# Kernel optimization log

Hardware: AMD Instinct MI355X
Metric: run time of the kernel (lower is better)

## Reference

```python
import jax, jax.numpy as jnp
import numpy as np

N_TAPS = 5
N_DELAY = 1
N_ITER = 2
REF_MIC = 0
EPS = 1e-3        # eps passed to ISS updates / divisions
MODEL_EPS = 1e-5  # LaplaceModel internal eps
PB_EPS = 1e-6     # projection_back eps


def _mag_sq(x):
    return jnp.real(x) ** 2 + jnp.imag(x) ** 2


def _div(num, den, eps=EPS):
    # torchiva divide: num / clamp(den, min=eps); den is real
    return num / jnp.maximum(den, eps)


def _laplace_model(Y):
    # Laplace source model: per-source/per-frame weight 1/(2*||y(:,n)||), broadcast over freq
    denom = 2.0 * jnp.sqrt(jnp.sum(_mag_sq(Y), axis=-2, keepdims=True))
    return jnp.broadcast_to(1.0 / jnp.maximum(denom, MODEL_EPS), Y.shape)


def _demix_derev(X, X_bar, W, H):
    reverb = jnp.einsum('...cfdt,...dftn->...cfn', H, X_bar)
    sep = jnp.einsum('...cfd,...dfn->...cfn', W, X)
    return sep - reverb


def _background_update(W, H, C_XX, C_XbarX):
    n_src = W.shape[-3]
    A = (jnp.einsum('...sfc,...cfd->...fsd', W, C_XX)
         + jnp.einsum('...sfdt,...dtfc->...fsc', H, C_XbarX))
    J_H = jnp.linalg.solve(A[..., :n_src], A[..., n_src:])  # (..., f, s, c-s)
    return jnp.moveaxis(jnp.conj(J_H), -1, -3)              # (..., c-s, f, s)


def _demix_background(X, J):
    n_src = J.shape[-1]
    return jnp.einsum('...cfd,...dfn->...cfn', J, X[..., :n_src, :, :]) - X[..., n_src:, :, :]


def _iss_v1(src, X, weights, eps=EPS):
    n_frames = X.shape[-1]
    Xs = X[..., src, :, :]
    v_num = jnp.einsum('...cfn,...cfn,...fn->...cf', weights, X, jnp.conj(Xs)) / n_frames
    v_den = jnp.einsum('...cfn,...fn->...cf', weights, _mag_sq(Xs)) / n_frames
    v = _div(v_num, v_den, eps)
    v_s = 1.0 - 1.0 / jnp.sqrt(jnp.maximum(v_den[..., src, :], eps))
    return v.at[..., src, :].set(v_s.astype(v.dtype))


def _iss_v23(X, Zs, weights, eps=EPS):
    v_num = jnp.einsum('...cfn,...cfn,...fn->...cf', weights, X, jnp.conj(Zs))
    v_den = jnp.einsum('...cfn,...fn->...cf', weights, _mag_sq(Zs))
    return _div(v_num, v_den, eps)


def _iss_updates_with_H(X, X_bar, W, H, weights, J=None, Z=None, eps=EPS):
    n_src = X.shape[-3]
    n_chan = n_src if J is None else n_src + Z.shape[-3]
    n_taps = X_bar.shape[-2]
    # sequential rank-1 source updates (loop-carried; small fixed trip count)
    for src in range(n_src):
        v = _iss_v1(src, X, weights, eps)
        X = X - jnp.einsum('...cf,...fn->...cfn', v, X[..., src, :, :])
        W = W - jnp.einsum('...cf,...fd->...cfd', v, W[..., src, :, :])
        H = H - jnp.einsum('...cf,...fdt->...cfdt', v, H[..., src, :, :, :])
    if Z is not None and J is not None:
        for bak in range(n_chan - n_src):
            v = _iss_v23(X, Z[..., bak, :, :], weights, eps)
            X = X - jnp.einsum('...cf,...fn->...cfn', v, Z[..., bak, :, :])
            W = W.at[..., :n_src].add(-jnp.einsum('...cf,...fd->...cfd', v, J[..., bak, :, :]))
            W = W.at[..., n_src + bak].add(v)
    for src in range(n_chan):
        for tap in range(n_taps):
            Xst = X_bar[..., src, :, tap, :]
            v = _iss_v23(X, Xst, weights, eps)
            X = X - jnp.einsum('...cf,...fn->...cfn', v, Xst)
            H = H.at[..., src, tap].add(v)
    return X, W, H


def _one_iter(Y, X, X_bar, C_XX, C_XbarX, W, H, J, eps=EPS):
    weights = _laplace_model(Y)
    g = jnp.maximum(jnp.mean(_mag_sq(Y), axis=(-2, -1), keepdims=True), eps)
    g_sqrt = jnp.sqrt(g)
    Y = _div(Y, g_sqrt, eps)
    W = _div(W, g_sqrt, eps)
    H = _div(H, g_sqrt[..., None], eps)
    weights = weights * g
    J = _background_update(W, H, C_XX, C_XbarX)
    Z = _demix_background(X, J)
    Y, W, H = _iss_updates_with_H(Y, X_bar, W, H, weights, J=J, Z=Z, eps=eps)
    return Y, W, H, J


def _projection_back(Y, W, J, ref_mic=REF_MIC, eps=PB_EPS):
    # overdetermined branch (n_src < n_chan), ref_mic < n_src
    n_src = Y.shape[-3]
    eye = jnp.eye(n_src, dtype=W.dtype)
    W1, W2 = W[..., :n_src], W[..., n_src:]
    B = jnp.einsum('...sfc,...cfk->...sfk', W2, J) + W1  # (..., s, f, s)
    rhs = eye[:, ref_mic:ref_mic + 1]                    # (s, 1)
    BT = jnp.einsum('...sfc->...fcs', B)                 # (..., f, s, s)
    rhs_b = jnp.broadcast_to(rhs, BT.shape[:-2] + rhs.shape)
    a = jnp.linalg.solve(BT + eps * eye, rhs_b)          # (..., f, s, 1)
    a = jnp.swapaxes(a, -3, -2)                          # (..., s, f, 1)
    return Y * a


def _forward(X, n_src):
    n_chan, n_freq, n_frames = X.shape[-3:]
    batch = X.shape[:-3]
    # delayed copies: X_bar[..., c, f, t, n] = X_pad[..., c, f, n + t]
    X_pad = jnp.pad(X, [(0, 0)] * (X.ndim - 1) + [(N_TAPS + N_DELAY, 0)])
    X_bar = jnp.stack([X_pad[..., t:t + n_frames] for t in range(N_TAPS)], axis=-2)
    C_XX = jnp.einsum('...cfn,...dfn->...cfd', X, jnp.conj(X)) / n_frames
    C_XbarX = jnp.einsum('...dftn,...cfn->...dtfc', X_bar, jnp.conj(X)) / n_frames
    eye = jnp.eye(n_chan, dtype=X.dtype)[:n_src]
    W = jnp.broadcast_to(eye[:, None, :], batch + (n_src, n_freq, n_chan))
    H = jnp.zeros(batch + (n_src, n_freq, n_chan, N_TAPS), dtype=X.dtype)
    J = jnp.zeros(batch + (n_chan - n_src, n_freq, n_src), dtype=X.dtype)
    Y = X[..., :n_src, :, :]
    for _ in range(N_ITER):
        Y, W, H, J = _one_iter(Y, X, X_bar, C_XX, C_XbarX, W, H, J)
    J = _background_update(W, H, C_XX, C_XbarX)
    Y = _demix_derev(X, X_bar, W, H)
    Y = _projection_back(Y, W, J)
    return Y


def setup_inputs():
    key = jax.random.key(0)
    k1, k2 = jax.random.split(key)
    B, n_chan, n_freq, n_frames = 2, 6, 257, 1000
    X_real = jax.random.normal(k1, (B, n_chan, n_freq, n_frames), dtype=jnp.float32)
    X_imag = jax.random.normal(k2, (B, n_chan, n_freq, n_frames), dtype=jnp.float32)
    return {"X_real": X_real, "X_imag": X_imag, "n_src": 2}


def reference(X_real, X_imag, n_src):
    X = jax.lax.complex(X_real, X_imag)
    Y = _forward(X, n_src)  # (B, n_src, n_freq, n_frames) complex
    # real view of the complex output: last axis = (real, imag)
    return jnp.stack([jnp.real(Y), jnp.imag(Y)], axis=-1)
```

## Files before the change

### kernel.cpp

```cpp
#include <hip/hip_runtime.h>
#include <math.h>

#define F_   257
#define N_   1000
#define C_   6
#define S_   2
#define K_   4
#define T_   5
#define DLY  6
#define EPSF 1e-3f
#define MODEL_EPSF 1e-5f
#define PB_EPSD 1e-6
#define NTHR 512

__device__ __forceinline__ float2 cmul(float2 a, float2 b){
  return make_float2(a.x*b.x - a.y*b.y, a.x*b.y + a.y*b.x);
}
__device__ __forceinline__ float2 cadd(float2 a, float2 b){ return make_float2(a.x+b.x, a.y+b.y); }
__device__ __forceinline__ float2 csub(float2 a, float2 b){ return make_float2(a.x-b.x, a.y-b.y); }

struct dc { double x, y; };
__device__ __forceinline__ dc dmul(dc a, dc b){ return dc{a.x*b.x - a.y*b.y, a.x*b.y + a.y*b.x}; }
__device__ __forceinline__ dc dadd(dc a, dc b){ return dc{a.x+b.x, a.y+b.y}; }
__device__ __forceinline__ dc dsub(dc a, dc b){ return dc{a.x-b.x, a.y-b.y}; }
__device__ __forceinline__ dc ddiv(dc a, dc b){
  double d = b.x*b.x + b.y*b.y;
  return dc{(a.x*b.x + a.y*b.y)/d, (a.y*b.x - a.x*b.y)/d};
}
__device__ __forceinline__ dc d_of(float2 a){ return dc{(double)a.x, (double)a.y}; }

struct V2 { float2 v0, v1; };

__global__ __launch_bounds__(512) void k_init(const float* __restrict__ Xre,
    const float* __restrict__ Xim, float2* __restrict__ Cxxg, float2* __restrict__ Cbxg)
{
  __shared__ float2 Xl[C_*N_];
  int p = blockIdx.x; int b = p / F_; int f = p - b*F_;
  int tid = threadIdx.x;

  for (int i = tid; i < C_*N_; i += NTHR){
    int c = i / N_, n = i - c*N_;
    size_t gi = ((size_t)(b*C_+c)*F_ + f)*N_ + n;
    Xl[i] = make_float2(Xre[gi], Xim[gi]);
  }
  __syncthreads();

  int wid = tid >> 6, lane = tid & 63;
  const float inv_n = 1.0f / (float)N_;
  for (int e = wid; e < 216; e += 8){
    int a_ch, b_ch, lag; float2* outp;
    if (e < 36){
      a_ch = e / 6; b_ch = e - a_ch*6; lag = 0;
      outp = &Cxxg[((size_t)p*C_ + a_ch)*C_ + b_ch];
    } else {
      int i2 = e - 36;
      int d = i2 / (T_*C_); int t = (i2 / C_) % T_; int c2 = i2 % C_;
      a_ch = d; b_ch = c2; lag = DLY - t;
      outp = &Cbxg[(((size_t)p*C_ + d)*T_ + t)*C_ + c2];
    }
    float accx = 0.f, accy = 0.f;
    for (int n = lane; n < N_; n += 64){
      if (n >= lag){
        float2 xa = Xl[a_ch*N_ + n - lag];
        float2 xb = Xl[b_ch*N_ + n];
        accx += xa.x*xb.x + xa.y*xb.y;
        accy += xa.y*xb.x - xa.x*xb.y;
      }
    }
    #pragma unroll
    for (int off = 32; off; off >>= 1){
      accx += __shfl_xor(accx, off);
      accy += __shfl_xor(accy, off);
    }
    if (lane == 0) *outp = make_float2(accx*inv_n, accy*inv_n);
  }
}

__global__ __launch_bounds__(128) void k_weights_x(const float* __restrict__ Xre,
    const float* __restrict__ Xim, float* __restrict__ deng, float* __restrict__ gsumg)
{
  __shared__ float redw[2];
  int blk = blockIdx.x;
  int fc = blk & 3; int ch = (blk >> 2) & 7; int s = (blk >> 5) & 1; int b = blk >> 6;
  int tid = threadIdx.x;
  int n = ch*125 + tid;
  int f0 = fc*65, f1 = (f0 + 65 < F_) ? f0 + 65 : F_;
  float acc = 0.f;
  if (tid < 125){
    for (int f = f0; f < f1; ++f){
      size_t gi = ((size_t)(b*C_+s)*F_ + f)*N_ + n;
      float xr = Xre[gi], xi = Xim[gi];
      acc += xr*xr + xi*xi;
    }
    atomicAdd(&deng[(b*S_+s)*N_ + n], acc);
  }
  float r = (tid < 125) ? acc : 0.f;
  #pragma unroll
  for (int off = 32; off; off >>= 1) r += __shfl_xor(r, off);
  if ((tid & 63) == 0) redw[tid >> 6] = r;
  __syncthreads();
  if (tid == 0) atomicAdd(&gsumg[b*S_+s], redw[0] + redw[1]);
}

__global__ __launch_bounds__(128) void k_weights_y(const float2* __restrict__ Yg,
    float* __restrict__ deng, float* __restrict__ gsumg)
{
  __shared__ float redw[2];
  int blk = blockIdx.x;
  int fc = blk & 3; int ch = (blk >> 2) & 7; int s = (blk >> 5) & 1; int b = blk >> 6;
  int tid = threadIdx.x;
  int n = ch*125 + tid;
  int f0 = fc*65, f1 = (f0 + 65 < F_) ? f0 + 65 : F_;
  float acc = 0.f;
  if (tid < 125){
    for (int f = f0; f < f1; ++f){
      float2 y = Yg[(((size_t)(b*F_+f))*S_ + s)*N_ + n];
      acc += y.x*y.x + y.y*y.y;
    }
    atomicAdd(&deng[(b*S_+s)*N_ + n], acc);
  }
  float r = (tid < 125) ? acc : 0.f;
  #pragma unroll
  for (int off = 32; off; off >>= 1) r += __shfl_xor(r, off);
  if ((tid & 63) == 0) redw[tid >> 6] = r;
  __syncthreads();
  if (tid == 0) atomicAdd(&gsumg[b*S_+s], redw[0] + redw[1]);
}

__device__ __forceinline__ void bg_update(int tid, int p, const float2* Wl,
    const float2* Hl, float2* Al, float2* Jl,
    const float2* __restrict__ Cxxg, const float2* __restrict__ Cbxg)
{
  if (tid < S_*C_){
    int s = tid / C_, j = tid - s*C_;
    float2 a = make_float2(0.f, 0.f);
    const float2* cx = Cxxg + (size_t)p*C_*C_;
    #pragma unroll
    for (int i = 0; i < C_; ++i) a = cadd(a, cmul(Wl[s*C_+i], cx[i*C_+j]));
    const float2* cb = Cbxg + (size_t)p*C_*T_*C_;
    #pragma unroll
    for (int i = 0; i < C_; ++i)
      #pragma unroll
      for (int t = 0; t < T_; ++t)
        a = cadd(a, cmul(Hl[(s*C_+i)*T_+t], cb[(i*T_+t)*C_+j]));
    Al[s*C_+j] = a;
  }
  __syncthreads();
  if (tid == 0){
    dc M00 = d_of(Al[0]),  M01 = d_of(Al[1]);
    dc M10 = d_of(Al[C_]), M11 = d_of(Al[C_+1]);
    dc det = dsub(dmul(M00, M11), dmul(M01, M10));
    #pragma unroll
    for (int k = 0; k < K_; ++k){
      dc r0 = d_of(Al[2+k]), r1 = d_of(Al[C_+2+k]);
      dc x0 = ddiv(dsub(dmul(M11, r0), dmul(M01, r1)), det);
      dc x1 = ddiv(dsub(dmul(M00, r1), dmul(M10, r0)), det);
      Jl[k*S_+0] = make_float2((float)x0.x, (float)(-x0.y));
      Jl[k*S_+1] = make_float2((float)x1.x, (float)(-x1.y));
    }
  }
  __syncthreads();
}

template<typename FS>
__device__ __forceinline__ V2 round2(int tid, bool hasB, int rb, float2* redv,
    float2& yA0, float2& yA1, float2& yB0, float2& yB1,
    float wA0, float wA1, float wB0, float wB1,
    FS sf, bool isV1, int src)
{
  float2 sA = sf(0), sB = sf(1);
  float m = sA.x*sA.x + sA.y*sA.y;
  float r0 = wA0*(yA0.x*sA.x + yA0.y*sA.y);
  float r1 = wA0*(yA0.y*sA.x - yA0.x*sA.y);
  float r2 = wA0*m;
  float r3 = wA1*(yA1.x*sA.x + yA1.y*sA.y);
  float r4 = wA1*(yA1.y*sA.x - yA1.x*sA.y);
  float r5 = wA1*m;
  if (hasB){
    float mb = sB.x*sB.x + sB.y*sB.y;
    r0 += wB0*(yB0.x*sB.x + yB0.y*sB.y);
    r1 += wB0*(yB0.y*sB.x - yB0.x*sB.y);
    r2 += wB0*mb;
    r3 += wB1*(yB1.x*sB.x + yB1.y*sB.y);
    r4 += wB1*(yB1.y*sB.x - yB1.x*sB.y);
    r5 += wB1*mb;
  }
  #pragma unroll
  for (int off = 32; off; off >>= 1){
    r0 += __shfl_xor(r0, off); r1 += __shfl_xor(r1, off);
    r2 += __shfl_xor(r2, off); r3 += __shfl_xor(r3, off);
    r4 += __shfl_xor(r4, off); r5 += __shfl_xor(r5, off);
  }
  if ((tid & 63) == 0){
    float2* rw = redv + rb*24 + (tid >> 6)*3;
    rw[0] = make_float2(r0, r1);
    rw[1] = make_float2(r2, r3);
    rw[2] = make_float2(r4, r5);
  }
  __syncthreads();
  const float2* rp = redv + rb*24;
  float t0=0,t1=0,t2=0,t3=0,t4=0,t5=0;
  #pragma unroll
  for (int w = 0; w < 8; ++w){
    float2 a = rp[w*3], b2 = rp[w*3+1], c2 = rp[w*3+2];
    t0 += a.x; t1 += a.y; t2 += b2.x; t3 += b2.y; t4 += c2.x; t5 += c2.y;
  }
  if (isV1){
    const float inv = 1.f/(float)N_;
    t0*=inv; t1*=inv; t2*=inv; t3*=inv; t4*=inv; t5*=inv;
  }
  float d0 = fmaxf(t2, EPSF), d1 = fmaxf(t5, EPSF);
  float2 v0 = make_float2(t0/d0, t1/d0);
  float2 v1 = make_float2(t3/d1, t4/d1);
  if (isV1){
    if (src == 0) v0 = make_float2(1.f - 1.f/sqrtf(d0), 0.f);
    else          v1 = make_float2(1.f - 1.f/sqrtf(d1), 0.f);
  }
  yA0 = csub(yA0, cmul(v0, sA)); yA1 = csub(yA1, cmul(v1, sA));
  if (hasB){ yB0 = csub(yB0, cmul(v0, sB)); yB1 = csub(yB1, cmul(v1, sB)); }
  return V2{v0, v1};
}

template<bool FIRST, bool FINAL>
__global__ __launch_bounds__(512, 4) void k_main(const float* __restrict__ Xre,
    const float* __restrict__ Xim, float2* __restrict__ Yg, float2* __restrict__ Wg,
    float2* __restrict__ Hg, const float2* __restrict__ Cxxg,
    const float2* __restrict__ Cbxg, const float* __restrict__ deng,
    const float* __restrict__ gsumg, float2* __restrict__ out2, int P)
{
  __shared__ float2 Xl[C_*N_];
  __shared__ float2 Wl[S_*C_];
  __shared__ float2 Hl[S_*C_*T_];
  __shared__ float2 Jl[K_*S_];
  __shared__ float2 Al[S_*C_];
  __shared__ float2 redv[2*8*3];

  int tid = threadIdx.x;
  const int nA = tid;
  const int nB = tid + NTHR;
  const bool hasB = (nB < N_);
  const int nBs = hasB ? nB : 0;

  for (int p = blockIdx.x; p < P; p += gridDim.x){
    __syncthreads();
    int b = p / F_, f = p - b*F_;

    for (int i = tid; i < C_*N_; i += NTHR){
      int c = i / N_, n = i - c*N_;
      size_t gi = ((size_t)(b*C_+c)*F_ + f)*N_ + n;
      Xl[i] = make_float2(Xre[gi], Xim[gi]);
    }

    float gv0 = fmaxf(gsumg[b*S_+0] * (1.f/((float)F_*(float)N_)), EPSF);
    float gv1 = fmaxf(gsumg[b*S_+1] * (1.f/((float)F_*(float)N_)), EPSF);
    float ig0 = 1.f / fmaxf(sqrtf(gv0), EPSF);
    float ig1 = 1.f / fmaxf(sqrtf(gv1), EPSF);

    float wA0 = gv0 / fmaxf(2.f*sqrtf(deng[(b*S_+0)*N_+nA]), MODEL_EPSF);
    float wA1 = gv1 / fmaxf(2.f*sqrtf(deng[(b*S_+1)*N_+nA]), MODEL_EPSF);
    float wB0 = 0.f, wB1 = 0.f;
    if (hasB){
      wB0 = gv0 / fmaxf(2.f*sqrtf(deng[(b*S_+0)*N_+nB]), MODEL_EPSF);
      wB1 = gv1 / fmaxf(2.f*sqrtf(deng[(b*S_+1)*N_+nB]), MODEL_EPSF);
    }

    if (FIRST){
      if (tid < S_*C_){
        int s = tid / C_, c = tid - s*C_;
        Wl[tid] = make_float2((s==c) ? (s ? ig1 : ig0) : 0.f, 0.f);
      }
      if (tid < S_*C_*T_) Hl[tid] = make_float2(0.f, 0.f);
    } else {
      if (tid < S_*C_){
        float ig = (tid / C_) ? ig1 : ig0;
        float2 w = Wg[(size_t)p*S_*C_ + tid];
        Wl[tid] = make_float2(w.x*ig, w.y*ig);
      }
      if (tid < S_*C_*T_){
        float ig = (tid / (C_*T_)) ? ig1 : ig0;
        float2 h = Hg[(size_t)p*S_*C_*T_ + tid];
        Hl[tid] = make_float2(h.x*ig, h.y*ig);
      }
    }
    __syncthreads();

    float2 xA0 = Xl[nA], xA1 = Xl[N_+nA];
    float2 xB0 = make_float2(0.f,0.f), xB1 = make_float2(0.f,0.f);
    if (hasB){ xB0 = Xl[nB]; xB1 = Xl[N_+nB]; }

    float2 yA0, yA1, yB0 = make_float2(0.f,0.f), yB1 = make_float2(0.f,0.f);
    if (FIRST){
      yA0 = make_float2(xA0.x*ig0, xA0.y*ig0);
      yA1 = make_float2(xA1.x*ig1, xA1.y*ig1);
      if (hasB){
        yB0 = make_float2(xB0.x*ig0, xB0.y*ig0);
        yB1 = make_float2(xB1.x*ig1, xB1.y*ig1);
      }
    } else {
      float2 t0 = Yg[((size_t)p*S_+0)*N_+nA];
      float2 t1 = Yg[((size_t)p*S_+1)*N_+nA];
      yA0 = make_float2(t0.x*ig0, t0.y*ig0);
      yA1 = make_float2(t1.x*ig1, t1.y*ig1);
      if (hasB){
        float2 u0 = Yg[((size_t)p*S_+0)*N_+nB];
        float2 u1 = Yg[((size_t)p*S_+1)*N_+nB];
        yB0 = make_float2(u0.x*ig0, u0.y*ig0);
        yB1 = make_float2(u1.x*ig1, u1.y*ig1);
      }
    }

    bg_update(tid, p, Wl, Hl, Al, Jl, Cxxg, Cbxg);

    int rr = 0;

    for (int src2 = 0; src2 < S_; ++src2){
      V2 v = round2(tid, hasB, (rr++)&1, redv, yA0,yA1,yB0,yB1, wA0,wA1,wB0,wB1,
          [&](int k)->float2 {
            return (src2 == 0) ? (k ? yB0 : yA0) : (k ? yB1 : yA1);
          }, true, src2);
      if (tid < C_){
        float2 ws = Wl[src2*C_+tid];
        Wl[tid]      = csub(Wl[tid],      cmul(v.v0, ws));
        Wl[C_+tid]   = csub(Wl[C_+tid],   cmul(v.v1, ws));
      } else if (tid >= 64 && tid < 64 + C_*T_){
        int i = tid - 64;
        float2 hs = Hl[src2*C_*T_+i];
        Hl[i]        = csub(Hl[i],        cmul(v.v0, hs));
        Hl[C_*T_+i]  = csub(Hl[C_*T_+i],  cmul(v.v1, hs));
      }
    }

    for (int bak = 0; bak < K_; ++bak){
      float2 J0 = Jl[bak*S_+0], J1 = Jl[bak*S_+1];
      V2 v = round2(tid, hasB, (rr++)&1, redv, yA0,yA1,yB0,yB1, wA0,wA1,wB0,wB1,
          [&](int k)->float2 {
            float2 x0 = k ? xB0 : xA0;
            float2 x1 = k ? xB1 : xA1;
            int n = k ? nBs : nA;
            float2 z = cadd(cmul(J0, x0), cmul(J1, x1));
            return csub(z, Xl[(S_+bak)*N_ + n]);
          }, false, 0);
      if (tid < S_){
        float2 vv = tid ? v.v1 : v.v0;
        Wl[tid*C_+0]      = csub(Wl[tid*C_+0], cmul(vv, J0));
        Wl[tid*C_+1]      = csub(Wl[tid*C_+1], cmul(vv, J1));
        Wl[tid*C_+S_+bak] = cadd(Wl[tid*C_+S_+bak], vv);
      }
    }

    for (int sc = 0; sc < C_; ++sc){
      for (int tap = 0; tap < T_; ++tap){
        int lag = DLY - tap;
        V2 v = round2(tid, hasB, (rr++)&1, redv, yA0,yA1,yB0,yB1, wA0,wA1,wB0,wB1,
            [&](int k)->float2 {
              int n = (k ? nBs : nA) - lag;
              return (n >= 0) ? Xl[sc*N_ + n] : make_float2(0.f, 0.f);
            }, false, 0);
        if (tid < S_){
          int idx = (tid*C_+sc)*T_+tap;
          Hl[idx] = cadd(Hl[idx], tid ? v.v1 : v.v0);
        }
      }
    }

    __syncthreads();

    if (!FINAL){
      Yg[((size_t)p*S_+0)*N_+nA] = yA0;
      Yg[((size_t)p*S_+1)*N_+nA] = yA1;
      if (hasB){
        Yg[((size_t)p*S_+0)*N_+nB] = yB0;
        Yg[((size_t)p*S_+1)*N_+nB] = yB1;
      }
      if (tid < S_*C_)    Wg[(size_t)p*S_*C_ + tid]    = Wl[tid];
      if (tid < S_*C_*T_) Hg[(size_t)p*S_*C_*T_ + tid] = Hl[tid];
    } else {
      bg_update(tid, p, Wl, Hl, Al, Jl, Cxxg, Cbxg);

      float2 oA0 = make_float2(0.f,0.f), oA1 = oA0, oB0 = oA0, oB1 = oA0;
      #pragma unroll
      for (int d = 0; d < C_; ++d){
        float2 x = Xl[d*N_+nA];
        oA0 = cadd(oA0, cmul(Wl[d],    x));
        oA1 = cadd(oA1, cmul(Wl[C_+d], x));
      }
      #pragma unroll
      for (int t = 0; t < T_; ++t){
        int m = nA - (DLY - t);
        if (m >= 0){
          #pragma unroll
          for (int d = 0; d < C_; ++d){
            float2 x = Xl[d*N_+m];
            oA0 = csub(oA0, cmul(Hl[d*T_+t],        x));
            oA1 = csub(oA1, cmul(Hl[(C_+d)*T_+t],   x));
          }
        }
      }
      if (hasB){
        #pragma unroll
        for (int d = 0; d < C_; ++d){
          float2 x = Xl[d*N_+nB];
          oB0 = cadd(oB0, cmul(Wl[d],    x));
          oB1 = cadd(oB1, cmul(Wl[C_+d], x));
        }
        #pragma unroll
        for (int t = 0; t < T_; ++t){
          int m = nB - (DLY - t);
          #pragma unroll
          for (int d = 0; d < C_; ++d){
            float2 x = Xl[d*N_+m];
            oB0 = csub(oB0, cmul(Hl[d*T_+t],      x));
            oB1 = csub(oB1, cmul(Hl[(C_+d)*T_+t], x));
          }
        }
      }

      if (tid == 0){
        dc Bm[2][2];
        #pragma unroll
        for (int s2 = 0; s2 < S_; ++s2)
          #pragma unroll
          for (int k = 0; k < S_; ++k){
            dc acc = d_of(Wl[s2*C_+k]);
            #pragma unroll
            for (int c = 0; c < K_; ++c)
              acc = dadd(acc, dmul(d_of(Wl[s2*C_+S_+c]), d_of(Jl[c*S_+k])));
            Bm[s2][k] = acc;
          }
        dc G00 = dc{Bm[0][0].x + PB_EPSD, Bm[0][0].y};
        dc G01 = Bm[1][0];
        dc G10 = Bm[0][1];
        dc G11 = dc{Bm[1][1].x + PB_EPSD, Bm[1][1].y};
        dc det = dsub(dmul(G00, G11), dmul(G01, G10));
        dc a0 = ddiv(G11, det);
        dc a1 = ddiv(dc{-G10.x, -G10.y}, det);
        Al[0] = make_float2((float)a0.x, (float)a0.y);
        Al[1] = make_float2((float)a1.x, (float)a1.y);
      }
      __syncthreads();
      float2 s0 = Al[0], s1 = Al[1];
      out2[((size_t)(b*S_+0)*F_ + f)*N_ + nA] = cmul(oA0, s0);
      out2[((size_t)(b*S_+1)*F_ + f)*N_ + nA] = cmul(oA1, s1);
      if (hasB){
        out2[((size_t)(b*S_+0)*F_ + f)*N_ + nB] = cmul(oB0, s0);
        out2[((size_t)(b*S_+1)*F_ + f)*N_ + nB] = cmul(oB1, s1);
      }
    }
  }
}

extern "C" void kernel_launch(void* const* d_in, const int* in_sizes, int n_in,
                              void* d_out, int out_size, void* d_ws, size_t ws_size,
                              hipStream_t stream)
{
  const float* Xre = (const float*)d_in[0];
  const float* Xim = (const float*)d_in[1];
  int B = in_sizes[0] / (C_*F_*N_);
  int P = B*F_;

  float2* Yg   = (float2*)d_ws;
  float2* Wg   = Yg   + (size_t)P*S_*N_;
  float2* Hg   = Wg   + (size_t)P*S_*C_;
  float2* Cxxg = Hg   + (size_t)P*S_*C_*T_;
  float2* Cbxg = Cxxg + (size_t)P*C_*C_;
  float*  deng = (float*)(Cbxg + (size_t)P*C_*T_*C_);
  float*  gsumg= deng + (size_t)B*S_*N_;
  float2* out2 = (float2*)d_out;

  size_t denBytes = ((size_t)B*S_*N_ + (size_t)B*S_) * sizeof(float);
  int G = (P < 512) ? P : 512;
  int WG = B*S_*8*4;

  hipMemsetAsync(deng, 0, denBytes, stream);
  k_weights_x<<<WG, 128, 0, stream>>>(Xre, Xim, deng, gsumg);
  k_init<<<P, 512, 0, stream>>>(Xre, Xim, Cxxg, Cbxg);
  k_main<true,false><<<G, 512, 0, stream>>>(Xre, Xim, Yg, Wg, Hg, Cxxg, Cbxg,
                                            deng, gsumg, nullptr, P);
  hipMemsetAsync(deng, 0, denBytes, stream);
  k_weights_y<<<WG, 128, 0, stream>>>(Yg, deng, gsumg);
  k_main<false,true><<<G, 512, 0, stream>>>(Xre, Xim, Yg, Wg, Hg, Cxxg, Cbxg,
                                            deng, gsumg, out2, P);
}
```

Baseline: 498.4 us.

## Fuse covariance init into first main pass and restructure launches

Removes the separate covariance kernel and computes Cxx/Cbx inside the first k_main pass from the already-loaded shared X tile, keeping them in shared memory and writing them to global memory for the second pass. k_main now launches one block per frequency bin instead of a grid-stride loop, with launch bounds raised to 6 waves. The weight kernels split frequency into 16 chunks for more blocks, the two denominator buffers are zeroed with a single memset, and the block-level reduction in round2 uses wave shuffles instead of a serial loop. Together these avoid a second global read of X, one kernel launch and one memset, at the cost of more shared memory and register pressure per block.

New measurement: 440.1 us. 1.13x faster.

```diff
diff --git a/kernel.cpp b/kernel.cpp
--- a/kernel.cpp
+++ b/kernel.cpp
@@ -31,60 +31,15 @@
 
 struct V2 { float2 v0, v1; };
 
-__global__ __launch_bounds__(512) void k_init(const float* __restrict__ Xre,
-    const float* __restrict__ Xim, float2* __restrict__ Cxxg, float2* __restrict__ Cbxg)
-{
-  __shared__ float2 Xl[C_*N_];
-  int p = blockIdx.x; int b = p / F_; int f = p - b*F_;
-  int tid = threadIdx.x;
-
-  for (int i = tid; i < C_*N_; i += NTHR){
-    int c = i / N_, n = i - c*N_;
-    size_t gi = ((size_t)(b*C_+c)*F_ + f)*N_ + n;
-    Xl[i] = make_float2(Xre[gi], Xim[gi]);
-  }
-  __syncthreads();
-
-  int wid = tid >> 6, lane = tid & 63;
-  const float inv_n = 1.0f / (float)N_;
-  for (int e = wid; e < 216; e += 8){
-    int a_ch, b_ch, lag; float2* outp;
-    if (e < 36){
-      a_ch = e / 6; b_ch = e - a_ch*6; lag = 0;
-      outp = &Cxxg[((size_t)p*C_ + a_ch)*C_ + b_ch];
-    } else {
-      int i2 = e - 36;
-      int d = i2 / (T_*C_); int t = (i2 / C_) % T_; int c2 = i2 % C_;
-      a_ch = d; b_ch = c2; lag = DLY - t;
-      outp = &Cbxg[(((size_t)p*C_ + d)*T_ + t)*C_ + c2];
-    }
-    float accx = 0.f, accy = 0.f;
-    for (int n = lane; n < N_; n += 64){
-      if (n >= lag){
-        float2 xa = Xl[a_ch*N_ + n - lag];
-        float2 xb = Xl[b_ch*N_ + n];
-        accx += xa.x*xb.x + xa.y*xb.y;
-        accy += xa.y*xb.x - xa.x*xb.y;
-      }
-    }
-    #pragma unroll
-    for (int off = 32; off; off >>= 1){
-      accx += __shfl_xor(accx, off);
-      accy += __shfl_xor(accy, off);
-    }
-    if (lane == 0) *outp = make_float2(accx*inv_n, accy*inv_n);
-  }
-}
-
 __global__ __launch_bounds__(128) void k_weights_x(const float* __restrict__ Xre,
     const float* __restrict__ Xim, float* __restrict__ deng, float* __restrict__ gsumg)
 {
   __shared__ float redw[2];
   int blk = blockIdx.x;
-  int fc = blk & 3; int ch = (blk >> 2) & 7; int s = (blk >> 5) & 1; int b = blk >> 6;
+  int fc = blk & 15; int ch = (blk >> 4) & 7; int s = (blk >> 7) & 1; int b = blk >> 8;
   int tid = threadIdx.x;
   int n = ch*125 + tid;
-  int f0 = fc*65, f1 = (f0 + 65 < F_) ? f0 + 65 : F_;
+  int f0 = fc*17, f1 = (f0 + 17 < F_) ? f0 + 17 : F_;
   float acc = 0.f;
   if (tid < 125){
     for (int f = f0; f < f1; ++f){
@@ -107,10 +62,10 @@
 {
   __shared__ float redw[2];
   int blk = blockIdx.x;
-  int fc = blk & 3; int ch = (blk >> 2) & 7; int s = (blk >> 5) & 1; int b = blk >> 6;
+  int fc = blk & 15; int ch = (blk >> 4) & 7; int s = (blk >> 7) & 1; int b = blk >> 8;
   int tid = threadIdx.x;
   int n = ch*125 + tid;
-  int f0 = fc*65, f1 = (f0 + 65 < F_) ? f0 + 65 : F_;
+  int f0 = fc*17, f1 = (f0 + 17 < F_) ? f0 + 17 : F_;
   float acc = 0.f;
   if (tid < 125){
     for (int f = f0; f < f1; ++f){
@@ -127,17 +82,15 @@
   if (tid == 0) atomicAdd(&gsumg[b*S_+s], redw[0] + redw[1]);
 }
 
-__device__ __forceinline__ void bg_update(int tid, int p, const float2* Wl,
+__device__ __forceinline__ void bg_update(int tid, const float2* Wl,
     const float2* Hl, float2* Al, float2* Jl,
-    const float2* __restrict__ Cxxg, const float2* __restrict__ Cbxg)
+    const float2* cx, const float2* cb)
 {
   if (tid < S_*C_){
     int s = tid / C_, j = tid - s*C_;
     float2 a = make_float2(0.f, 0.f);
-    const float2* cx = Cxxg + (size_t)p*C_*C_;
     #pragma unroll
     for (int i = 0; i < C_; ++i) a = cadd(a, cmul(Wl[s*C_+i], cx[i*C_+j]));
-    const float2* cb = Cbxg + (size_t)p*C_*T_*C_;
     #pragma unroll
     for (int i = 0; i < C_; ++i)
       #pragma unroll
@@ -163,7 +116,7 @@
 }
 
 template<typename FS>
-__device__ __forceinline__ V2 round2(int tid, bool hasB, int rb, float2* redv,
+__device__ __forceinline__ V2 round2(int tid, bool hasB, int rb, float* redl,
     float2& yA0, float2& yA1, float2& yB0, float2& yB1,
     float wA0, float wA1, float wB0, float wB1,
     FS sf, bool isV1, int src)
@@ -191,20 +144,20 @@
     r2 += __shfl_xor(r2, off); r3 += __shfl_xor(r3, off);
     r4 += __shfl_xor(r4, off); r5 += __shfl_xor(r5, off);
   }
-  if ((tid & 63) == 0){
-    float2* rw = redv + rb*24 + (tid >> 6)*3;
+  int lane = tid & 63, wid = tid >> 6;
+  if (lane == 0){
+    float2* rw = (float2*)(redl + rb*64 + wid*8);
     rw[0] = make_float2(r0, r1);
     rw[1] = make_float2(r2, r3);
     rw[2] = make_float2(r4, r5);
   }
   __syncthreads();
-  const float2* rp = redv + rb*24;
-  float t0=0,t1=0,t2=0,t3=0,t4=0,t5=0;
-  #pragma unroll
-  for (int w = 0; w < 8; ++w){
-    float2 a = rp[w*3], b2 = rp[w*3+1], c2 = rp[w*3+2];
-    t0 += a.x; t1 += a.y; t2 += b2.x; t3 += b2.y; t4 += c2.x; t5 += c2.y;
-  }
+  float pv = ((lane & 7) < 6) ? redl[rb*64 + (lane >> 3)*8 + (lane & 7)] : 0.f;
+  pv += __shfl_xor(pv, 8);
+  pv += __shfl_xor(pv, 16);
+  pv += __shfl_xor(pv, 32);
+  float t0 = __shfl(pv, 0), t1 = __shfl(pv, 1), t2 = __shfl(pv, 2);
+  float t3 = __shfl(pv, 3), t4 = __shfl(pv, 4), t5 = __shfl(pv, 5);
   if (isV1){
     const float inv = 1.f/(float)N_;
     t0*=inv; t1*=inv; t2*=inv; t3*=inv; t4*=inv; t5*=inv;
@@ -222,229 +175,265 @@
 }
 
 template<bool FIRST, bool FINAL>
-__global__ __launch_bounds__(512, 4) void k_main(const float* __restrict__ Xre,
+__global__ __launch_bounds__(512, 6) void k_main(const float* __restrict__ Xre,
     const float* __restrict__ Xim, float2* __restrict__ Yg, float2* __restrict__ Wg,
-    float2* __restrict__ Hg, const float2* __restrict__ Cxxg,
-    const float2* __restrict__ Cbxg, const float* __restrict__ deng,
-    const float* __restrict__ gsumg, float2* __restrict__ out2, int P)
+    float2* __restrict__ Hg, float2* __restrict__ Cxxg,
+    float2* __restrict__ Cbxg, const float* __restrict__ deng,
+    const float* __restrict__ gsumg, float2* __restrict__ out2)
 {
   __shared__ float2 Xl[C_*N_];
   __shared__ float2 Wl[S_*C_];
   __shared__ float2 Hl[S_*C_*T_];
   __shared__ float2 Jl[K_*S_];
   __shared__ float2 Al[S_*C_];
-  __shared__ float2 redv[2*8*3];
-
+  __shared__ float  redl[2*64];
+  __shared__ float2 Cxl[C_*C_];
+  __shared__ float2 Cbl[C_*T_*C_];
+
+  int p = blockIdx.x; int b = p / F_; int f = p - b*F_;
   int tid = threadIdx.x;
   const int nA = tid;
   const int nB = tid + NTHR;
   const bool hasB = (nB < N_);
   const int nBs = hasB ? nB : 0;
 
-  for (int p = blockIdx.x; p < P; p += gridDim.x){
+  for (int i = tid; i < C_*N_; i += NTHR){
+    int c = i / N_, n = i - c*N_;
+    size_t gi = ((size_t)(b*C_+c)*F_ + f)*N_ + n;
+    Xl[i] = make_float2(Xre[gi], Xim[gi]);
+  }
+  if (tid < 128) redl[tid] = 0.f;
+
+  float gv0 = fmaxf(gsumg[b*S_+0] * (1.f/((float)F_*(float)N_)), EPSF);
+  float gv1 = fmaxf(gsumg[b*S_+1] * (1.f/((float)F_*(float)N_)), EPSF);
+  float ig0 = 1.f / fmaxf(sqrtf(gv0), EPSF);
+  float ig1 = 1.f / fmaxf(sqrtf(gv1), EPSF);
+
+  float wA0 = gv0 / fmaxf(2.f*sqrtf(deng[(b*S_+0)*N_+nA]), MODEL_EPSF);
+  float wA1 = gv1 / fmaxf(2.f*sqrtf(deng[(b*S_+1)*N_+nA]), MODEL_EPSF);
+  float wB0 = 0.f, wB1 = 0.f;
+  if (hasB){
+    wB0 = gv0 / fmaxf(2.f*sqrtf(deng[(b*S_+0)*N_+nB]), MODEL_EPSF);
+    wB1 = gv1 / fmaxf(2.f*sqrtf(deng[(b*S_+1)*N_+nB]), MODEL_EPSF);
+  }
+
+  if (FIRST){
+    if (tid < S_*C_){
+      int s = tid / C_, c = tid - s*C_;
+      Wl[tid] = make_float2((s==c) ? (s ? ig1 : ig0) : 0.f, 0.f);
+    }
+    if (tid < S_*C_*T_) Hl[tid] = make_float2(0.f, 0.f);
+  } else {
+    if (tid < S_*C_){
+      float ig = (tid / C_) ? ig1 : ig0;
+      float2 w = Wg[(size_t)p*S_*C_ + tid];
+      Wl[tid] = make_float2(w.x*ig, w.y*ig);
+    }
+    if (tid < S_*C_*T_){
+      float ig = (tid / (C_*T_)) ? ig1 : ig0;
+      float2 h = Hg[(size_t)p*S_*C_*T_ + tid];
+      Hl[tid] = make_float2(h.x*ig, h.y*ig);
+    }
+  }
+  __syncthreads();
+
+  if (FIRST){
+    int wid = tid >> 6, lane = tid & 63;
+    const float inv_n = 1.0f / (float)N_;
+    for (int e = wid; e < 216; e += 8){
+      int a_ch, b_ch, lag;
+      if (e < 36){ a_ch = e / 6; b_ch = e - a_ch*6; lag = 0; }
+      else {
+        int i2 = e - 36;
+        a_ch = i2 / (T_*C_); int t = (i2 / C_) % T_; b_ch = i2 % C_;
+        lag = DLY - t;
+      }
+      float accx = 0.f, accy = 0.f;
+      for (int n = lane; n < N_; n += 64){
+        if (n >= lag){
+          float2 xa = Xl[a_ch*N_ + n - lag];
+          float2 xb = Xl[b_ch*N_ + n];
+          accx += xa.x*xb.x + xa.y*xb.y;
+          accy += xa.y*xb.x - xa.x*xb.y;
+        }
+      }
+      #pragma unroll
+      for (int off = 32; off; off >>= 1){
+        accx += __shfl_xor(accx, off);
+        accy += __shfl_xor(accy, off);
+      }
+      if (lane == 0){
+        float2 r = make_float2(accx*inv_n, accy*inv_n);
+        if (e < 36){ Cxl[e] = r; Cxxg[(size_t)p*(C_*C_) + e] = r; }
+        else { Cbl[e-36] = r; Cbxg[(size_t)p*(C_*T_*C_) + (e-36)] = r; }
+      }
+    }
     __syncthreads();
-    int b = p / F_, f = p - b*F_;
-
-    for (int i = tid; i < C_*N_; i += NTHR){
-      int c = i / N_, n = i - c*N_;
-      size_t gi = ((size_t)(b*C_+c)*F_ + f)*N_ + n;
-      Xl[i] = make_float2(Xre[gi], Xim[gi]);
-    }
-
-    float gv0 = fmaxf(gsumg[b*S_+0] * (1.f/((float)F_*(float)N_)), EPSF);
-    float gv1 = fmaxf(gsumg[b*S_+1] * (1.f/((float)F_*(float)N_)), EPSF);
-    float ig0 = 1.f / fmaxf(sqrtf(gv0), EPSF);
-    float ig1 = 1.f / fmaxf(sqrtf(gv1), EPSF);
-
-    float wA0 = gv0 / fmaxf(2.f*sqrtf(deng[(b*S_+0)*N_+nA]), MODEL_EPSF);
-    float wA1 = gv1 / fmaxf(2.f*sqrtf(deng[(b*S_+1)*N_+nA]), MODEL_EPSF);
-    float wB0 = 0.f, wB1 = 0.f;
+  }
+
+  const float2* cx = FIRST ? (const float2*)Cxl : (const float2*)(Cxxg + (size_t)p*C_*C_);
+  const float2* cb = FIRST ? (const float2*)Cbl : (const float2*)(Cbxg + (size_t)p*C_*T_*C_);
+
+  float2 xA0 = Xl[nA], xA1 = Xl[N_+nA];
+  float2 xB0 = make_float2(0.f,0.f), xB1 = make_float2(0.f,0.f);
+  if (hasB){ xB0 = Xl[nB]; xB1 = Xl[N_+nB]; }
+
+  float2 yA0, yA1, yB0 = make_float2(0.f,0.f), yB1 = make_float2(0.f,0.f);
+  if (FIRST){
+    yA0 = make_float2(xA0.x*ig0, xA0.y*ig0);
+    yA1 = make_float2(xA1.x*ig1, xA1.y*ig1);
     if (hasB){
-      wB0 = gv0 / fmaxf(2.f*sqrtf(deng[(b*S_+0)*N_+nB]), MODEL_EPSF);
-      wB1 = gv1 / fmaxf(2.f*sqrtf(deng[(b*S_+1)*N_+nB]), MODEL_EPSF);
-    }
-
-    if (FIRST){
-      if (tid < S_*C_){
-        int s = tid / C_, c = tid - s*C_;
-        Wl[tid] = make_float2((s==c) ? (s ? ig1 : ig0) : 0.f, 0.f);
-      }
-      if (tid < S_*C_*T_) Hl[tid] = make_float2(0.f, 0.f);
-    } else {
-      if (tid < S_*C_){
-        float ig = (tid / C_) ? ig1 : ig0;
-        float2 w = Wg[(size_t)p*S_*C_ + tid];
-        Wl[tid] = make_float2(w.x*ig, w.y*ig);
-      }
-      if (tid < S_*C_*T_){
-        float ig = (tid / (C_*T_)) ? ig1 : ig0;
-        float2 h = Hg[(size_t)p*S_*C_*T_ + tid];
-        Hl[tid] = make_float2(h.x*ig, h.y*ig);
-      }
-    }
-    __syncthreads();
-
-    float2 xA0 = Xl[nA], xA1 = Xl[N_+nA];
-    float2 xB0 = make_float2(0.f,0.f), xB1 = make_float2(0.f,0.f);
-    if (hasB){ xB0 = Xl[nB]; xB1 = Xl[N_+nB]; }
-
-    float2 yA0, yA1, yB0 = make_float2(0.f,0.f), yB1 = make_float2(0.f,0.f);
-    if (FIRST){
-      yA0 = make_float2(xA0.x*ig0, xA0.y*ig0);
-      yA1 = make_float2(xA1.x*ig1, xA1.y*ig1);
-      if (hasB){
-        yB0 = make_float2(xB0.x*ig0, xB0.y*ig0);
-        yB1 = make_float2(xB1.x*ig1, xB1.y*ig1);
-      }
-    } else {
-      float2 t0 = Yg[((size_t)p*S_+0)*N_+nA];
-      float2 t1 = Yg[((size_t)p*S_+1)*N_+nA];
-      yA0 = make_float2(t0.x*ig0, t0.y*ig0);
-      yA1 = make_float2(t1.x*ig1, t1.y*ig1);
-      if (hasB){
-        float2 u0 = Yg[((size_t)p*S_+0)*N_+nB];
-        float2 u1 = Yg[((size_t)p*S_+1)*N_+nB];
-        yB0 = make_float2(u0.x*ig0, u0.y*ig0);
-        yB1 = make_float2(u1.x*ig1, u1.y*ig1);
-      }
-    }
-
-    bg_update(tid, p, Wl, Hl, Al, Jl, Cxxg, Cbxg);
-
-    int rr = 0;
-
-    for (int src2 = 0; src2 < S_; ++src2){
-      V2 v = round2(tid, hasB, (rr++)&1, redv, yA0,yA1,yB0,yB1, wA0,wA1,wB0,wB1,
+      yB0 = make_float2(xB0.x*ig0, xB0.y*ig0);
+      yB1 = make_float2(xB1.x*ig1, xB1.y*ig1);
+    }
+  } else {
+    float2 t0 = Yg[((size_t)p*S_+0)*N_+nA];
+    float2 t1 = Yg[((size_t)p*S_+1)*N_+nA];
+    yA0 = make_float2(t0.x*ig0, t0.y*ig0);
+    yA1 = make_float2(t1.x*ig1, t1.y*ig1);
+    if (hasB){
+      float2 u0 = Yg[((size_t)p*S_+0)*N_+nB];
+      float2 u1 = Yg[((size_t)p*S_+1)*N_+nB];
+      yB0 = make_float2(u0.x*ig0, u0.y*ig0);
+      yB1 = make_float2(u1.x*ig1, u1.y*ig1);
+    }
+  }
+
+  bg_update(tid, Wl, Hl, Al, Jl, cx, cb);
+
+  int rr = 0;
+
+  for (int src2 = 0; src2 < S_; ++src2){
+    V2 v = round2(tid, hasB, (rr++)&1, redl, yA0,yA1,yB0,yB1, wA0,wA1,wB0,wB1,
+        [&](int k)->float2 {
+          return (src2 == 0) ? (k ? yB0 : yA0) : (k ? yB1 : yA1);
+        }, true, src2);
+    if (tid < C_){
+      float2 ws = Wl[src2*C_+tid];
+      Wl[tid]      = csub(Wl[tid],      cmul(v.v0, ws));
+      Wl[C_+tid]   = csub(Wl[C_+tid],   cmul(v.v1, ws));
+    } else if (tid >= 64 && tid < 64 + C_*T_){
+      int i = tid - 64;
+      float2 hs = Hl[src2*C_*T_+i];
+      Hl[i]        = csub(Hl[i],        cmul(v.v0, hs));
+      Hl[C_*T_+i]  = csub(Hl[C_*T_+i],  cmul(v.v1, hs));
+    }
+  }
+
+  for (int bak = 0; bak < K_; ++bak){
+    float2 J0 = Jl[bak*S_+0], J1 = Jl[bak*S_+1];
+    V2 v = round2(tid, hasB, (rr++)&1, redl, yA0,yA1,yB0,yB1, wA0,wA1,wB0,wB1,
+        [&](int k)->float2 {
+          float2 x0 = k ? xB0 : xA0;
+          float2 x1 = k ? xB1 : xA1;
+          int n = k ? nBs : nA;
+          float2 z = cadd(cmul(J0, x0), cmul(J1, x1));
+          return csub(z, Xl[(S_+bak)*N_ + n]);
+        }, false, 0);
+    if (tid < S_){
+      float2 vv = tid ? v.v1 : v.v0;
+      Wl[tid*C_+0]      = csub(Wl[tid*C_+0], cmul(vv, J0));
+      Wl[tid*C_+1]      = csub(Wl[tid*C_+1], cmul(vv, J1));
+      Wl[tid*C_+S_+bak] = cadd(Wl[tid*C_+S_+bak], vv);
+    }
+  }
+
+  for (int sc = 0; sc < C_; ++sc){
+    for (int tap = 0; tap < T_; ++tap){
+      int lag = DLY - tap;
+      V2 v = round2(tid, hasB, (rr++)&1, redl, yA0,yA1,yB0,yB1, wA0,wA1,wB0,wB1,
           [&](int k)->float2 {
-            return (src2 == 0) ? (k ? yB0 : yA0) : (k ? yB1 : yA1);
-          }, true, src2);
-      if (tid < C_){
-        float2 ws = Wl[src2*C_+tid];
-        Wl[tid]      = csub(Wl[tid],      cmul(v.v0, ws));
-        Wl[C_+tid]   = csub(Wl[C_+tid],   cmul(v.v1, ws));
-      } else if (tid >= 64 && tid < 64 + C_*T_){
-        int i = tid - 64;
-        float2 hs = Hl[src2*C_*T_+i];
-        Hl[i]        = csub(Hl[i],        cmul(v.v0, hs));
-        Hl[C_*T_+i]  = csub(Hl[C_*T_+i],  cmul(v.v1, hs));
-      }
-    }
-
-    for (int bak = 0; bak < K_; ++bak){
-      float2 J0 = Jl[bak*S_+0], J1 = Jl[bak*S_+1];
-      V2 v = round2(tid, hasB, (rr++)&1, redv, yA0,yA1,yB0,yB1, wA0,wA1,wB0,wB1,
-          [&](int k)->float2 {
-            float2 x0 = k ? xB0 : xA0;
-            float2 x1 = k ? xB1 : xA1;
-            int n = k ? nBs : nA;
-            float2 z = cadd(cmul(J0, x0), cmul(J1, x1));
-            return csub(z, Xl[(S_+bak)*N_ + n]);
+            int n = (k ? nBs : nA) - lag;
+            return (n >= 0) ? Xl[sc*N_ + n] : make_float2(0.f, 0.f);
           }, false, 0);
       if (tid < S_){
-        float2 vv = tid ? v.v1 : v.v0;
-        Wl[tid*C_+0]      = csub(Wl[tid*C_+0], cmul(vv, J0));
-        Wl[tid*C_+1]      = csub(Wl[tid*C_+1], cmul(vv, J1));
-        Wl[tid*C_+S_+bak] = cadd(Wl[tid*C_+S_+bak], vv);
-      }
-    }
-
-    for (int sc = 0; sc < C_; ++sc){
-      for (int tap = 0; tap < T_; ++tap){
-        int lag = DLY - tap;
-        V2 v = round2(tid, hasB, (rr++)&1, redv, yA0,yA1,yB0,yB1, wA0,wA1,wB0,wB1,
-            [&](int k)->float2 {
-              int n = (k ? nBs : nA) - lag;
-              return (n >= 0) ? Xl[sc*N_ + n] : make_float2(0.f, 0.f);
-            }, false, 0);
-        if (tid < S_){
-          int idx = (tid*C_+sc)*T_+tap;
-          Hl[idx] = cadd(Hl[idx], tid ? v.v1 : v.v0);
+        int idx = (tid*C_+sc)*T_+tap;
+        Hl[idx] = cadd(Hl[idx], tid ? v.v1 : v.v0);
+      }
+    }
+  }
+
+  __syncthreads();
+
+  if (!FINAL){
+    Yg[((size_t)p*S_+0)*N_+nA] = yA0;
+    Yg[((size_t)p*S_+1)*N_+nA] = yA1;
+    if (hasB){
+      Yg[((size_t)p*S_+0)*N_+nB] = yB0;
+      Yg[((size_t)p*S_+1)*N_+nB] = yB1;
+    }
+    if (tid < S_*C_)    Wg[(size_t)p*S_*C_ + tid]    = Wl[tid];
+    if (tid < S_*C_*T_) Hg[(size_t)p*S_*C_*T_ + tid] = Hl[tid];
+  } else {
+    bg_update(tid, Wl, Hl, Al, Jl, cx, cb);
+
+    float2 oA0 = make_float2(0.f,0.f), oA1 = oA0, oB0 = oA0, oB1 = oA0;
+    #pragma unroll
+    for (int d = 0; d < C_; ++d){
+      float2 x = Xl[d*N_+nA];
+      oA0 = cadd(oA0, cmul(Wl[d],    x));
+      oA1 = cadd(oA1, cmul(Wl[C_+d], x));
+    }
+    #pragma unroll
+    for (int t = 0; t < T_; ++t){
+      int m = nA - (DLY - t);
+      if (m >= 0){
+        #pragma unroll
+        for (int d = 0; d < C_; ++d){
+          float2 x = Xl[d*N_+m];
+          oA0 = csub(oA0, cmul(Hl[d*T_+t],      x));
+          oA1 = csub(oA1, cmul(Hl[(C_+d)*T_+t], x));
         }
       }
     }
-
-    __syncthreads();
-
-    if (!FINAL){
-      Yg[((size_t)p*S_+0)*N_+nA] = yA0;
-      Yg[((size_t)p*S_+1)*N_+nA] = yA1;
-      if (hasB){
-        Yg[((size_t)p*S_+0)*N_+nB] = yB0;
-        Yg[((size_t)p*S_+1)*N_+nB] = yB1;
-      }
-      if (tid < S_*C_)    Wg[(size_t)p*S_*C_ + tid]    = Wl[tid];
-      if (tid < S_*C_*T_) Hg[(size_t)p*S_*C_*T_ + tid] = Hl[tid];
-    } else {
-      bg_update(tid, p, Wl, Hl, Al, Jl, Cxxg, Cbxg);
-
-      float2 oA0 = make_float2(0.f,0.f), oA1 = oA0, oB0 = oA0, oB1 = oA0;
+    if (hasB){
       #pragma unroll
       for (int d = 0; d < C_; ++d){
-        float2 x = Xl[d*N_+nA];
-        oA0 = cadd(oA0, cmul(Wl[d],    x));
-        oA1 = cadd(oA1, cmul(Wl[C_+d], x));
+        float2 x = Xl[d*N_+nB];
+        oB0 = cadd(oB0, cmul(Wl[d],    x));
+        oB1 = cadd(oB1, cmul(Wl[C_+d], x));
       }
       #pragma unroll
       for (int t = 0; t < T_; ++t){
-        int m = nA - (DLY - t);
-        if (m >= 0){
-          #pragma unroll
-          for (int d = 0; d < C_; ++d){
-            float2 x = Xl[d*N_+m];
-            oA0 = csub(oA0, cmul(Hl[d*T_+t],        x));
-            oA1 = csub(oA1, cmul(Hl[(C_+d)*T_+t],   x));
-          }
-        }
-      }
-      if (hasB){
+        int m = nB - (DLY - t);
         #pragma unroll
         for (int d = 0; d < C_; ++d){
-          float2 x = Xl[d*N_+nB];
-          oB0 = cadd(oB0, cmul(Wl[d],    x));
-          oB1 = cadd(oB1, cmul(Wl[C_+d], x));
+          float2 x = Xl[d*N_+m];
+          oB0 = csub(oB0, cmul(Hl[d*T_+t],      x));
+          oB1 = csub(oB1, cmul(Hl[(C_+d)*T_+t], x));
         }
+      }
+    }
+
+    if (tid == 0){
+      dc Bm[2][2];
+      #pragma unroll
+      for (int s2 = 0; s2 < S_; ++s2)
         #pragma unroll
-        for (int t = 0; t < T_; ++t){
-          int m = nB - (DLY - t);
+        for (int k = 0; k < S_; ++k){
+          dc acc = d_of(Wl[s2*C_+k]);
           #pragma unroll
-          for (int d = 0; d < C_; ++d){
-            float2 x = Xl[d*N_+m];
-            oB0 = csub(oB0, cmul(Hl[d*T_+t],      x));
-            oB1 = csub(oB1, cmul(Hl[(C_+d)*T_+t], x));
-          }
+          for (int c = 0; c < K_; ++c)
+            acc = dadd(acc, dmul(d_of(Wl[s2*C_+S_+c]), d_of(Jl[c*S_+k])));
+          Bm[s2][k] = acc;
         }
-      }
-
-      if (tid == 0){
-        dc Bm[2][2];
-        #pragma unroll
-        for (int s2 = 0; s2 < S_; ++s2)
-          #pragma unroll
-          for (int k = 0; k < S_; ++k){
-            dc acc = d_of(Wl[s2*C_+k]);
-            #pragma unroll
-            for (int c = 0; c < K_; ++c)
-              acc = dadd(acc, dmul(d_of(Wl[s2*C_+S_+c]), d_of(Jl[c*S_+k])));
-            Bm[s2][k] = acc;
-          }
-        dc G00 = dc{Bm[0][0].x + PB_EPSD, Bm[0][0].y};
-        dc G01 = Bm[1][0];
-        dc G10 = Bm[0][1];
-        dc G11 = dc{Bm[1][1].x + PB_EPSD, Bm[1][1].y};
-        dc det = dsub(dmul(G00, G11), dmul(G01, G10));
-        dc a0 = ddiv(G11, det);
-        dc a1 = ddiv(dc{-G10.x, -G10.y}, det);
-        Al[0] = make_float2((float)a0.x, (float)a0.y);
-        Al[1] = make_float2((float)a1.x, (float)a1.y);
-      }
-      __syncthreads();
-      float2 s0 = Al[0], s1 = Al[1];
-      out2[((size_t)(b*S_+0)*F_ + f)*N_ + nA] = cmul(oA0, s0);
-      out2[((size_t)(b*S_+1)*F_ + f)*N_ + nA] = cmul(oA1, s1);
-      if (hasB){
-        out2[((size_t)(b*S_+0)*F_ + f)*N_ + nB] = cmul(oB0, s0);
-        out2[((size_t)(b*S_+1)*F_ + f)*N_ + nB] = cmul(oB1, s1);
-      }
+      dc G00 = dc{Bm[0][0].x + PB_EPSD, Bm[0][0].y};
+      dc G01 = Bm[1][0];
+      dc G10 = Bm[0][1];
+      dc G11 = dc{Bm[1][1].x + PB_EPSD, Bm[1][1].y};
+      dc det = dsub(dmul(G00, G11), dmul(G01, G10));
+      dc a0 = ddiv(G11, det);
+      dc a1 = ddiv(dc{-G10.x, -G10.y}, det);
+      Al[0] = make_float2((float)a0.x, (float)a0.y);
+      Al[1] = make_float2((float)a1.x, (float)a1.y);
+    }
+    __syncthreads();
+    float2 s0 = Al[0], s1 = Al[1];
+    out2[((size_t)(b*S_+0)*F_ + f)*N_ + nA] = cmul(oA0, s0);
+    out2[((size_t)(b*S_+1)*F_ + f)*N_ + nA] = cmul(oA1, s1);
+    if (hasB){
+      out2[((size_t)(b*S_+0)*F_ + f)*N_ + nB] = cmul(oB0, s0);
+      out2[((size_t)(b*S_+1)*F_ + f)*N_ + nB] = cmul(oB1, s1);
     }
   }
 }
@@ -458,26 +447,25 @@
   int B = in_sizes[0] / (C_*F_*N_);
   int P = B*F_;
 
-  float2* Yg   = (float2*)d_ws;
-  float2* Wg   = Yg   + (size_t)P*S_*N_;
-  float2* Hg   = Wg   + (size_t)P*S_*C_;
-  float2* Cxxg = Hg   + (size_t)P*S_*C_*T_;
-  float2* Cbxg = Cxxg + (size_t)P*C_*C_;
-  float*  deng = (float*)(Cbxg + (size_t)P*C_*T_*C_);
-  float*  gsumg= deng + (size_t)B*S_*N_;
-  float2* out2 = (float2*)d_out;
-
-  size_t denBytes = ((size_t)B*S_*N_ + (size_t)B*S_) * sizeof(float);
-  int G = (P < 512) ? P : 512;
-  int WG = B*S_*8*4;
-
-  hipMemsetAsync(deng, 0, denBytes, stream);
-  k_weights_x<<<WG, 128, 0, stream>>>(Xre, Xim, deng, gsumg);
-  k_init<<<P, 512, 0, stream>>>(Xre, Xim, Cxxg, Cbxg);
-  k_main<true,false><<<G, 512, 0, stream>>>(Xre, Xim, Yg, Wg, Hg, Cxxg, Cbxg,
-                                            deng, gsumg, nullptr, P);
-  hipMemsetAsync(deng, 0, denBytes, stream);
-  k_weights_y<<<WG, 128, 0, stream>>>(Yg, deng, gsumg);
-  k_main<false,true><<<G, 512, 0, stream>>>(Xre, Xim, Yg, Wg, Hg, Cxxg, Cbxg,
-                                            deng, gsumg, out2, P);
-}
+  float2* Yg    = (float2*)d_ws;
+  float2* Wg    = Yg    + (size_t)P*S_*N_;
+  float2* Hg    = Wg    + (size_t)P*S_*C_;
+  float2* Cxxg  = Hg    + (size_t)P*S_*C_*T_;
+  float2* Cbxg  = Cxxg  + (size_t)P*C_*C_;
+  float*  deng0 = (float*)(Cbxg + (size_t)P*C_*T_*C_);
+  float*  deng1 = deng0 + (size_t)B*S_*N_;
+  float*  gsum0 = deng1 + (size_t)B*S_*N_;
+  float*  gsum1 = gsum0 + (size_t)B*S_;
+  float2* out2  = (float2*)d_out;
+
+  size_t zeroBytes = (2*(size_t)B*S_*N_ + 2*(size_t)B*S_) * sizeof(float);
+  int WG = B*S_*8*16;
+
+  hipMemsetAsync(deng0, 0, zeroBytes, stream);
+  k_weights_x<<<WG, 128, 0, stream>>>(Xre, Xim, deng0, gsum0);
+  k_main<true,false><<<P, 512, 0, stream>>>(Xre, Xim, Yg, Wg, Hg, Cxxg, Cbxg,
+                                            deng0, gsum0, nullptr);
+  k_weights_y<<<WG, 128, 0, stream>>>(Yg, deng1, gsum1);
+  k_main<false,true><<<P, 512, 0, stream>>>(Xre, Xim, Yg, Wg, Hg, Cxxg, Cbxg,
+                                            deng1, gsum1, out2);
+}
```
